# Performance work log

Hardware: AMD Instinct MI355X
Metric: run time of the kernel (lower is better)

Reference implementation:

```python
import jax, jax.numpy as jnp
import numpy as np

N_NODES = 100000
N_EDGES = 1600000
NFEAT = 128
NHID = 128
NCLASS = 40


def gcn_conv(x, W, b, src, dst, n_nodes):
    """PyG-style GCNConv: x' = D^{-1/2}(A+I)D^{-1/2} (x W) + b."""
    h = x @ W  # [N, out]
    loop = jnp.arange(n_nodes, dtype=src.dtype)
    s = jnp.concatenate([src, loop])  # add self-loops
    d = jnp.concatenate([dst, loop])
    deg = jax.ops.segment_sum(jnp.ones_like(s, dtype=h.dtype), d, num_segments=n_nodes)
    dinv = jnp.where(deg > 0, jax.lax.rsqrt(deg), 0.0)
    norm = dinv[s] * dinv[d]  # [E+N]
    msg = h[s] * norm[:, None]  # gather + scale
    out = jax.ops.segment_sum(msg, d, num_segments=n_nodes)  # scatter-add
    return out + b


def setup_inputs() -> dict:
    key = jax.random.key(0)
    ks = jax.random.split(key, 6)
    x = jax.random.normal(ks[0], (N_NODES, NFEAT), dtype=jnp.float32)
    edge_index = jax.random.randint(ks[1], (2, N_EDGES), 0, N_NODES, dtype=jnp.int64)
    sc1 = 1.0 / np.sqrt(NFEAT)
    sc2 = 1.0 / np.sqrt(NHID)
    W1 = jax.random.normal(ks[2], (NFEAT, NHID), dtype=jnp.float32) * sc1
    b1 = jnp.zeros((NHID,), dtype=jnp.float32)
    Wm = jax.random.normal(ks[3], (NHID, NHID), dtype=jnp.float32) * sc2
    bm = jnp.zeros((NHID,), dtype=jnp.float32)
    W2 = jax.random.normal(ks[4], (NHID, NCLASS), dtype=jnp.float32) * sc2
    b2 = jnp.zeros((NCLASS,), dtype=jnp.float32)
    return {"x": x, "edge_index": edge_index, "W1": W1, "b1": b1,
            "Wm": Wm, "bm": bm, "W2": W2, "b2": b2}


def reference(x, edge_index, W1, b1, Wm, bm, W2, b2):
    # StandGCNX forward, eval mode (dropout = identity)
    src, dst = edge_index[0], edge_index[1]
    n = x.shape[0]
    h = jax.nn.relu(gcn_conv(x, W1, b1, src, dst, n))
    h = jax.nn.relu(gcn_conv(h, Wm, bm, src, dst, n))
    out = gcn_conv(h, W2, b2, src, dst, n)
    return out
```

## Files before the change

kernel.cpp:

```cpp
#include <hip/hip_runtime.h>
#include <hip/hip_bf16.h>

typedef __attribute__((ext_vector_type(8))) short bf16x8;
typedef __attribute__((ext_vector_type(4))) float f32x4;

__device__ __forceinline__ ushort bf16rne(float f) {
    uint u = __float_as_uint(f);
    return (ushort)((u + 0x7fffu + ((u >> 16) & 1u)) >> 16);
}
__device__ __forceinline__ void unpack2(uint p, float& a, float& b) {
    a = __uint_as_float(p << 16);
    b = __uint_as_float(p & 0xffff0000u);
}


__global__ __launch_bounds__(256) void k_prep_pack(const float* __restrict__ W1,
                                                   const float* __restrict__ Wm,
                                                   const float* __restrict__ W2,
                                                   ushort* __restrict__ w1t,
                                                   ushort* __restrict__ wmt,
                                                   ushort* __restrict__ w2t,
                                                   const int* __restrict__ src,
                                                   const int* __restrict__ dst,
                                                   int* __restrict__ bcur,
                                                   uint* __restrict__ pairbuf,
                                                   int E, int nbuck, int CAP) {
    __shared__ int hist[512];
    __shared__ int scn[512];
    __shared__ int cur[512];
    __shared__ int gbase[512];
    __shared__ uint sorted[4096];
    int b = blockIdx.x;
    int t = threadIdx.x;
    if (b < 160) {
        if (b < 64) {
            int i = b * 256 + t; int k = i >> 7, n = i & 127;
            w1t[n * 128 + k] = bf16rne(W1[k * 128 + n]);
        } else if (b < 128) {
            int i = (b - 64) * 256 + t; int k = i >> 7, n = i & 127;
            wmt[n * 128 + k] = bf16rne(Wm[k * 128 + n]);
        } else {
            int i = (b - 128) * 256 + t;
            int n = i >> 7, k = i & 127;
            w2t[n * 128 + k] = (n < 40) ? bf16rne(W2[k * 40 + n]) : (ushort)0;
        }
        return;
    }
    int off = (b - 160) * 4096;
    int cnt = min(4096, E - off);
    hist[t] = 0; hist[t + 256] = 0;
    __syncthreads();
    for (int i = t; i < cnt; i += 256) {
        int bb = dst[off + i] >> 8;
        atomicAdd(&hist[bb], 1);
    }
    __syncthreads();
    scn[t] = hist[t]; scn[t + 256] = hist[t + 256];
    __syncthreads();
    for (int d = 1; d < 256; d <<= 1) {
        int u0 = (t >= d) ? scn[t - d] : 0;
        int u1 = (t >= d) ? scn[256 + t - d] : 0;
        __syncthreads();
        if (t >= d) { scn[t] += u0; scn[256 + t] += u1; }
        __syncthreads();
    }
    int tot0 = scn[255];
    scn[256 + t] += tot0;
    __syncthreads();
    cur[t] = (t == 0) ? 0 : scn[t - 1];
    cur[t + 256] = scn[t + 255];
    if (t < nbuck && hist[t] > 0)
        gbase[t] = t * CAP + atomicAdd(&bcur[t], hist[t]);
    int t2 = t + 256;
    if (t2 < nbuck && hist[t2] > 0)
        gbase[t2] = t2 * CAP + atomicAdd(&bcur[t2], hist[t2]);
    __syncthreads();
    for (int i = t; i < cnt; i += 256) {
        int d = dst[off + i];
        int s = src[off + i];
        int bb = d >> 8;
        int pos = atomicAdd(&cur[bb], 1);
        sorted[pos] = ((uint)(d & 255) << 24) | (uint)s;
    }
    __syncthreads();
    int wid = t >> 6, lane = t & 63;
    for (int bb = wid; bb < nbuck; bb += 4) {
        int n = hist[bb];
        if (n == 0) continue;
        int ls = (bb == 0) ? 0 : scn[bb - 1];
        int gb = gbase[bb];
        for (int j = lane; j < n; j += 64)
            pairbuf[gb + j] = sorted[ls + j];
    }
}


#define CSR_CAP 5632
__global__ __launch_bounds__(256) void k_csr_gemm(const uint* __restrict__ pairbuf,
                                                  const int* __restrict__ bcur,
                                                  int* __restrict__ rowptr,
                                                  int* __restrict__ rowend,
                                                  float* __restrict__ dinv,
                                                  int* __restrict__ csr,
                                                  int N, int nbuck, int CAP,
                                                  const float* __restrict__ A,
                                                  const ushort* __restrict__ Wt,
                                                  ushort* __restrict__ C, int M) {
    __shared__ int lhist[256];
    __shared__ int scn[256];
    __shared__ int lcur[256];
    __shared__ int lcsr[CSR_CAP];
    int t = threadIdx.x;
    if ((int)blockIdx.x >= nbuck) {
        int blk = blockIdx.x - nbuck;
        int wave = t >> 6, lane = t & 63;
        int m16 = lane & 15, quad = lane >> 4;
        int rowA = blk * 64 + wave * 16 + m16;
        int rA = min(rowA, M - 1);
        const float4* A4 = (const float4*)A;

        f32x4 acc[8];
#pragma unroll
        for (int i = 0; i < 8; i++) acc[i] = (f32x4){0.f, 0.f, 0.f, 0.f};
#pragma unroll
        for (int it = 0; it < 4; it++) {
            float4 f0 = A4[(size_t)rA * 32 + 8 * it + 2 * quad];
            float4 f1 = A4[(size_t)rA * 32 + 8 * it + 2 * quad + 1];
            bf16x8 af;
            af[0] = (short)bf16rne(f0.x); af[1] = (short)bf16rne(f0.y);
            af[2] = (short)bf16rne(f0.z); af[3] = (short)bf16rne(f0.w);
            af[4] = (short)bf16rne(f1.x); af[5] = (short)bf16rne(f1.y);
            af[6] = (short)bf16rne(f1.z); af[7] = (short)bf16rne(f1.w);
#pragma unroll
            for (int nt = 0; nt < 8; nt++) {
                bf16x8 bfr = *(const bf16x8*)(Wt + (size_t)(nt * 16 + m16) * 128 + it * 32 + quad * 8);
                acc[nt] = __builtin_amdgcn_mfma_f32_16x16x32_bf16(af, bfr, acc[nt], 0, 0, 0);
            }
        }
        int rowBase = blk * 64 + wave * 16 + quad * 4;
#pragma unroll
        for (int nt = 0; nt < 8; nt++) {
            int col = nt * 16 + m16;
#pragma unroll
            for (int r = 0; r < 4; r++) {
                int row = rowBase + r;
                if (row < M) C[(size_t)row * 128 + col] = bf16rne(acc[nt][r]);
            }
        }
        return;
    }
    int b = blockIdx.x;
    int base = b << 8;
    int nn = min(256, N - base);
    int lo = b * CAP;
    int cnt = bcur[b];
    lhist[t] = 0;
    __syncthreads();
    for (int i = t; i < cnt; i += 256) atomicAdd(&lhist[pairbuf[lo + i] >> 24], 1);
    __syncthreads();
    int mydeg = lhist[t];
    scn[t] = mydeg;
    __syncthreads();
    for (int d = 1; d < 256; d <<= 1) {
        int u = (t >= d) ? scn[t - d] : 0;
        __syncthreads();
        if (t >= d) scn[t] += u;
        __syncthreads();
    }
    int excl = (t == 0) ? 0 : scn[t - 1];
    lcur[t] = excl;
    if (t < nn) {
        rowptr[base + t] = lo + excl;
        rowend[base + t] = lo + excl + mydeg;
        dinv[base + t] = rsqrtf((float)(mydeg + 1));
    }
    __syncthreads();
    if (cnt <= CSR_CAP) {
        for (int i = t; i < cnt; i += 256) {
            uint p = pairbuf[lo + i];
            int pos = atomicAdd(&lcur[p >> 24], 1);
            lcsr[pos] = (int)(p & 0xFFFFFFu);
        }
        __syncthreads();
        for (int i = t; i < cnt; i += 256) csr[lo + i] = lcsr[i];
    } else {
        for (int i = t; i < cnt; i += 256) {
            uint p = pairbuf[lo + i];
            int pos = lo + atomicAdd(&lcur[p >> 24], 1);
            csr[pos] = (int)(p & 0xFFFFFFu);
        }
    }
}


template <bool EDGE_W>
__device__ __forceinline__ void batch8(const uint* __restrict__ g32, int lane,
                                       int creg, int wreg, int j, int lim,
                                       float& x0, float& x1) {
    uint P[8]; float W[8];
#pragma unroll
    for (int k = 0; k < 8; k++) {
        int idx = j + k;
        int cl = idx < 63 ? idx : 63;
        int s = __builtin_amdgcn_readlane(creg, cl);
        float w = EDGE_W ? __int_as_float(__builtin_amdgcn_readlane(wreg, cl)) : 1.0f;
        W[k] = (idx < lim) ? w : 0.0f;
        P[k] = g32[(size_t)s * 64 + lane];
    }
#pragma unroll
    for (int k = 0; k < 8; k++) {
        float u, v; unpack2(P[k], u, v);
        x0 += u * W[k]; x1 += v * W[k];
    }
}

template <bool EDGE_W>
__device__ __forceinline__ void batch8x2(const uint* __restrict__ g32, int lane,
                                         int cA, int wA, int jA, int limA,
                                         float& a0, float& a1,
                                         int cB, int wB, int jB, int limB,
                                         float& b0, float& b1) {
    uint PA[8], PB[8]; float WA[8], WB[8];
#pragma unroll
    for (int k = 0; k < 8; k++) {
        int idx = jA + k;
        int cl = idx < 63 ? idx : 63;
        int s = __builtin_amdgcn_readlane(cA, cl);
        float w = EDGE_W ? __int_as_float(__builtin_amdgcn_readlane(wA, cl)) : 1.0f;
        WA[k] = (idx < limA) ? w : 0.0f;
        PA[k] = g32[(size_t)s * 64 + lane];
    }
#pragma unroll
    for (int k = 0; k < 8; k++) {
        int idx = jB + k;
        int cl = idx < 63 ? idx : 63;
        int s = __builtin_amdgcn_readlane(cB, cl);
        float w = EDGE_W ? __int_as_float(__builtin_amdgcn_readlane(wB, cl)) : 1.0f;
        WB[k] = (idx < limB) ? w : 0.0f;
        PB[k] = g32[(size_t)s * 64 + lane];
    }
#pragma unroll
    for (int k = 0; k < 8; k++) {
        float u, v; unpack2(PA[k], u, v);
        a0 += u * WA[k]; a1 += v * WA[k];
    }
#pragma unroll
    for (int k = 0; k < 8; k++) {
        float u, v; unpack2(PB[k], u, v);
        b0 += u * WB[k]; b1 += v * WB[k];
    }
}

template <bool EDGE_W>
__device__ __forceinline__ void agg_node_chunked(const uint* __restrict__ g32,
                                                 const int* __restrict__ csr,
                                                 const float* __restrict__ dinv,
                                                 int lane, int e0, int e1,
                                                 float& x0, float& x1) {
    for (int base = e0; base < e1; base += 64) {
        int nc = e1 - base; if (nc > 64) nc = 64;
        int sidx = 0, swi = 0;
        if (lane < nc) {
            sidx = csr[base + lane];
            if (EDGE_W) swi = __float_as_int(dinv[sidx]);
        }
        int nc8 = (nc + 7) & ~7;
        for (int j = 0; j < nc8; j += 8)
            batch8<EDGE_W>(g32, lane, sidx, swi, j, nc, x0, x1);
    }
}

template <int NT, bool EDGE_W>
__device__ __forceinline__ void fused_agg_gemm(const ushort* __restrict__ g,
                                               const float* __restrict__ dinv,
                                               const int* __restrict__ rowptr,
                                               const int* __restrict__ rowend,
                                               const int* __restrict__ csr,
                                               const float* __restrict__ bias,
                                               const ushort* __restrict__ Wt,
                                               ushort* __restrict__ C,
                                               int M, int ccols) {
    __shared__ ushort hs[32][136];
    int t = threadIdx.x;
    int lane = t & 63;
    int wave = t >> 6;
    const uint* g32 = (const uint*)g;
    float2 bb = ((const float2*)bias)[lane];

    int nodeBase = blockIdx.x * 32 + wave * 8;
    int nd_l = min(nodeBase + lane, M - 1);

    uint srow[8];
#pragma unroll
    for (int i = 0; i < 8; i++) {
        int nd = __builtin_amdgcn_readlane(nd_l, i);
        srow[i] = g32[(size_t)nd * 64 + lane];
    }
    int e0_l = 0, e1_l = 0; float dn_l = 0.f;
    if (lane < 8) {
        e0_l = rowptr[nd_l];
        e1_l = rowend[nd_l];
        dn_l = dinv[nd_l];
    }
    int c0 = 0, c1 = 0, c2 = 0, c3 = 0;
    int w0 = 0, w1 = 0, w2 = 0, w3 = 0;
    int sp0, sp1, sp2, sp3, Ls0, Ls1, Ls2, Ls3;
    sp0 = __builtin_amdgcn_readlane(e0_l, 0);
    Ls0 = __builtin_amdgcn_readlane(e1_l, 1) - sp0;
    sp1 = __builtin_amdgcn_readlane(e0_l, 2);
    Ls1 = __builtin_amdgcn_readlane(e1_l, 3) - sp1;
    sp2 = __builtin_amdgcn_readlane(e0_l, 4);
    Ls2 = __builtin_amdgcn_readlane(e1_l, 5) - sp2;
    sp3 = __builtin_amdgcn_readlane(e0_l, 6);
    Ls3 = __builtin_amdgcn_readlane(e1_l, 7) - sp3;
    if (Ls0 > 0 && Ls0 <= 64 && lane < Ls0) c0 = csr[sp0 + lane];
    if (Ls1 > 0 && Ls1 <= 64 && lane < Ls1) c1 = csr[sp1 + lane];
    if (Ls2 > 0 && Ls2 <= 64 && lane < Ls2) c2 = csr[sp2 + lane];
    if (Ls3 > 0 && Ls3 <= 64 && lane < Ls3) c3 = csr[sp3 + lane];
    if (EDGE_W) {
        if (Ls0 > 0 && Ls0 <= 64 && lane < Ls0) w0 = __float_as_int(dinv[c0]);
        if (Ls1 > 0 && Ls1 <= 64 && lane < Ls1) w1 = __float_as_int(dinv[c1]);
        if (Ls2 > 0 && Ls2 <= 64 && lane < Ls2) w2 = __float_as_int(dinv[c2]);
        if (Ls3 > 0 && Ls3 <= 64 && lane < Ls3) w3 = __float_as_int(dinv[c3]);
    }
    int cp[4] = {c0, c1, c2, c3};
    int wp[4] = {w0, w1, w2, w3};
    int spp[4] = {sp0, sp1, sp2, sp3};
    int Lsp[4] = {Ls0, Ls1, Ls2, Ls3};

#pragma unroll
    for (int p = 0; p < 4; p++) {
        int iA = 2 * p, iB = 2 * p + 1;
        int eA0 = __builtin_amdgcn_readlane(e0_l, iA);
        int eA1 = __builtin_amdgcn_readlane(e1_l, iA);
        int eB0 = __builtin_amdgcn_readlane(e0_l, iB);
        int eB1 = __builtin_amdgcn_readlane(e1_l, iB);
        float dnA = __int_as_float(__builtin_amdgcn_readlane(__float_as_int(dn_l), iA));
        float dnB = __int_as_float(__builtin_amdgcn_readlane(__float_as_int(dn_l), iB));
        float a0, a1, b0, b1;
        {
            float u, v;
            unpack2(srow[2 * p], u, v);
            if (EDGE_W) { a0 = u * dnA; a1 = v * dnA; } else { a0 = u; a1 = v; }
            unpack2(srow[2 * p + 1], u, v);
            if (EDGE_W) { b0 = u * dnB; b1 = v * dnB; } else { b0 = u; b1 = v; }
        }
        if (Lsp[p] > 0 && Lsp[p] <= 64) {
            int offA = eA0 - spp[p];
            int offB = eB0 - spp[p];
            int nA = eA1 - eA0, nB = eB1 - eB0;
            int limA = offA + nA, limB = offB + nB;
            int jA = offA, jB = offB;
            int jAend = offA + ((nA + 7) & ~7);
            int jBend = offB + ((nB + 7) & ~7);
            while (jA < jAend && jB < jBend) {
                batch8x2<EDGE_W>(g32, lane, cp[p], wp[p], jA, limA, a0, a1,
                                 cp[p], wp[p], jB, limB, b0, b1);
                jA += 8; jB += 8;
            }
            while (jA < jAend) { batch8<EDGE_W>(g32, lane, cp[p], wp[p], jA, limA, a0, a1); jA += 8; }
            while (jB < jBend) { batch8<EDGE_W>(g32, lane, cp[p], wp[p], jB, limB, b0, b1); jB += 8; }
        } else if (Lsp[p] > 64) {
            agg_node_chunked<EDGE_W>(g32, csr, dinv, lane, eA0, eA1, a0, a1);
            agg_node_chunked<EDGE_W>(g32, csr, dinv, lane, eB0, eB1, b0, b1);
        }
        float o0 = fmaxf(a0 * dnA + bb.x, 0.f);
        float o1 = fmaxf(a1 * dnA + bb.y, 0.f);
        float o2 = fmaxf(b0 * dnB + bb.x, 0.f);
        float o3 = fmaxf(b1 * dnB + bb.y, 0.f);
        uint qA = (uint)bf16rne(o0) | ((uint)bf16rne(o1) << 16);
        uint qB = (uint)bf16rne(o2) | ((uint)bf16rne(o3) << 16);
        *(uint*)&hs[wave * 8 + 2 * p][lane * 2] = qA;
        *(uint*)&hs[wave * 8 + 2 * p + 1][lane * 2] = qB;
    }
    __syncthreads();

    int wv = t >> 6, lane6 = t & 63;
    int m16 = lane6 & 15, quad = lane6 >> 4;
    int rowHalf = wv & 1;
    int ntHalf = wv >> 1;
    constexpr int NTH = (NT + 1) / 2;
    int ntStart = ntHalf * NTH;
    int ntEnd = ntHalf ? NT : NTH;

    f32x4 acc[NTH];
#pragma unroll
    for (int i = 0; i < NTH; i++) acc[i] = (f32x4){0.f, 0.f, 0.f, 0.f};
#pragma unroll
    for (int it = 0; it < 4; it++) {
        bf16x8 af = *(const bf16x8*)&hs[rowHalf * 16 + m16][it * 32 + quad * 8];
        for (int nt = ntStart; nt < ntEnd; nt++) {
            bf16x8 bfr = *(const bf16x8*)(Wt + (size_t)(nt * 16 + m16) * 128 + it * 32 + quad * 8);
            acc[nt - ntStart] = __builtin_amdgcn_mfma_f32_16x16x32_bf16(af, bfr, acc[nt - ntStart], 0, 0, 0);
        }
    }
    int rowBase = blockIdx.x * 32 + rowHalf * 16 + quad * 4;
    float dnv[4];
#pragma unroll
    for (int r = 0; r < 4; r++) dnv[r] = dinv[min(rowBase + r, M - 1)];
    for (int nt = ntStart; nt < ntEnd; nt++) {
        int col = nt * 16 + m16;
        if (col >= ccols) continue;
#pragma unroll
        for (int r = 0; r < 4; r++) {
            int row = rowBase + r;
            if (row < M) C[(size_t)row * ccols + col] = bf16rne(acc[nt - ntStart][r] * dnv[r]);
        }
    }
}

__global__ __launch_bounds__(256) void k_fusedA(const ushort* __restrict__ g,
                                                const float* __restrict__ dinv,
                                                const int* __restrict__ rowptr,
                                                const int* __restrict__ rowend,
                                                const int* __restrict__ csr,
                                                const float* __restrict__ bias,
                                                const ushort* __restrict__ Wt,
                                                ushort* __restrict__ C, int M) {
    fused_agg_gemm<8, true>(g, dinv, rowptr, rowend, csr, bias, Wt, C, M, 128);
}

__global__ __launch_bounds__(256) void k_fusedB(const ushort* __restrict__ g,
                                                const float* __restrict__ dinv,
                                                const int* __restrict__ rowptr,
                                                const int* __restrict__ rowend,
                                                const int* __restrict__ csr,
                                                const float* __restrict__ bias,
                                                const ushort* __restrict__ Wt,
                                                ushort* __restrict__ C, int M) {
    fused_agg_gemm<4, false>(g, dinv, rowptr, rowend, csr, bias, Wt, C, M, 64);
}


__global__ __launch_bounds__(256) void k_agg40_b(const ushort* __restrict__ g3,
                                                 const float* __restrict__ dinv,
                                                 const int* __restrict__ rowptr,
                                                 const int* __restrict__ rowend,
                                                 const int* __restrict__ csr,
                                                 const float* __restrict__ bias,
                                                 float* __restrict__ out, int N) {
    int t = threadIdx.x;
    int wave = t >> 6, lane = t & 63;
    int half = lane >> 5, hl = lane & 31;
    const uint* gp = (const uint*)g3;

    int node0 = (blockIdx.x * 4 + wave) * 2;
    int nA = min(node0, N - 1);
    int nB = min(node0 + 1, N - 1);
    int myNode = half ? nB : nA;
    float dn = dinv[myNode];
    int e0A = rowptr[nA], e1A = rowend[nA];
    int e0B = rowptr[nB], e1B = rowend[nB];

    float a0, a1;
    {
        uint p = gp[(size_t)myNode * 32 + hl];
        unpack2(p, a0, a1);
    }
    int baseA = e0A, baseB = e0B;
    while (baseA < e1A || baseB < e1B) {
        int ncA = e1A - baseA; if (ncA > 32) ncA = 32; if (ncA < 0) ncA = 0;
        int ncB = e1B - baseB; if (ncB > 32) ncB = 32; if (ncB < 0) ncB = 0;
        int myBase = half ? baseB : baseA;
        int myNc = half ? ncB : ncA;
        int sidx = 0;
        if (hl < myNc) sidx = csr[myBase + hl];
        int lim = myNc;
        int m8A = (ncA + 7) & ~7;
        int m8B = (ncB + 7) & ~7;
        int m8 = m8A > m8B ? m8A : m8B;
        for (int j = 0; j < m8; j += 8) {
            uint P[8]; float W[8];
#pragma unroll
            for (int k = 0; k < 8; k++) {
                int idx = j + k;
                int cl = idx < 31 ? idx : 31;
                int sA = __builtin_amdgcn_readlane(sidx, cl);
                int sB = __builtin_amdgcn_readlane(sidx, 32 + cl);
                int s = half ? sB : sA;
                W[k] = (idx < lim) ? 1.0f : 0.0f;
                P[k] = gp[(size_t)s * 32 + hl];
            }
#pragma unroll
            for (int k = 0; k < 8; k++) {
                float u, v; unpack2(P[k], u, v);
                a0 += u * W[k]; a1 += v * W[k];
            }
        }
        baseA += ncA;
        baseB += ncB;
    }
    int onode = node0 + half;
    if (onode < N && hl < 20) {
        float2 bb = ((const float2*)bias)[hl];
        float2 o;
        o.x = a0 * dn + bb.x;
        o.y = a1 * dn + bb.y;
        ((float2*)out)[(size_t)onode * 20 + hl] = o;
    }
}


extern "C" void kernel_launch(void* const* d_in, const int* in_sizes, int n_in,
                              void* d_out, int out_size, void* d_ws, size_t ws_size,
                              hipStream_t stream) {
    const float* x  = (const float*)d_in[0];
    const int* eidx = (const int*)d_in[1];
    const float* W1 = (const float*)d_in[2];
    const float* b1 = (const float*)d_in[3];
    const float* Wm = (const float*)d_in[4];
    const float* bm = (const float*)d_in[5];
    const float* W2 = (const float*)d_in[6];
    const float* b2 = (const float*)d_in[7];
    float* out = (float*)d_out;

    int N = in_sizes[0] / 128;
    int E = in_sizes[1] / 2;
    const int* src = eidx;
    const int* dst = eidx + E;
    int nbuck = (N + 255) >> 8;
    int ntile = (E + 4095) / 4096;
    int CAP = ((E / nbuck) * 3 / 2 + 511) & ~511;

    char* ws = (char*)d_ws;
    size_t off = 0;
    auto alloc = [&](size_t bytes) -> void* {
        void* p = ws + off;
        off += (bytes + 255) & ~(size_t)255;
        return p;
    };
    float*  dinv    = (float*)alloc((size_t)N * 4);
    int*    rowptr  = (int*)alloc((size_t)N * 4);
    int*    rowend  = (int*)alloc((size_t)N * 4);
    int*    csr     = (int*)alloc((size_t)nbuck * CAP * 4);
    uint*   pairbuf = (uint*)alloc((size_t)nbuck * CAP * 4);
    int*    bcur    = (int*)alloc(512 * 4);
    ushort* w1t     = (ushort*)alloc(128 * 128 * 2);
    ushort* wmt     = (ushort*)alloc(128 * 128 * 2);
    ushort* w2t     = (ushort*)alloc(64 * 128 * 2);
    ushort* gbuf    = (ushort*)alloc((size_t)N * 128 * 2);
    ushort* gbuf2   = (ushort*)alloc((size_t)N * 128 * 2);
    ushort* g3      = (ushort*)alloc((size_t)N * 64 * 2);

    int gblk64 = (N + 63) / 64;
    int gblk32 = (N + 31) / 32;

    hipMemsetAsync(bcur, 0, 512 * 4, stream);
    k_prep_pack<<<160 + ntile, 256, 0, stream>>>(W1, Wm, W2, w1t, wmt, w2t,
                                                 src, dst, bcur, pairbuf, E, nbuck, CAP);
    k_csr_gemm<<<nbuck + gblk64, 256, 0, stream>>>(pairbuf, bcur, rowptr, rowend, dinv,
                                                   csr, N, nbuck, CAP, x, w1t, gbuf, N);
    k_fusedA<<<gblk32, 256, 0, stream>>>(gbuf, dinv, rowptr, rowend, csr, b1, wmt, gbuf2, N);
    k_fusedB<<<gblk32, 256, 0, stream>>>(gbuf2, dinv, rowptr, rowend, csr, bm, w2t, g3, N);
    k_agg40_b<<<(N + 7) / 8, 256, 0, stream>>>(g3, dinv, rowptr, rowend, csr, b2, out, N);
}
```

Measured before the change: 362.9 us.

## Prescale first GEMM output by source dinv to drop per-edge weights

Computes node degrees with global atomics during the edge bucketing pass and scales the first GEMM output rows by rsqrt(deg+1), so the layer-1 aggregation no longer needs to gather dinv per edge or multiply edge weights. Both fused aggregation kernels now use the unweighted path. This removes a random dinv gather and readlane per edge in layer 1, at the cost of 1.6M global atomics on deg and a larger memset.

New measurement: 418.1 us. 1.15x slower.

```diff
diff --git a/kernel.cpp b/kernel.cpp
--- a/kernel.cpp
+++ b/kernel.cpp
@@ -23,6 +23,7 @@
                                                    const int* __restrict__ src,
                                                    const int* __restrict__ dst,
                                                    int* __restrict__ bcur,
+                                                   int* __restrict__ deg,
                                                    uint* __restrict__ pairbuf,
                                                    int E, int nbuck, int CAP) {
     __shared__ int hist[512];
@@ -78,6 +79,7 @@
     for (int i = t; i < cnt; i += 256) {
         int d = dst[off + i];
         int s = src[off + i];
+        atomicAdd(&deg[d], 1);
         int bb = d >> 8;
         int pos = atomicAdd(&cur[bb], 1);
         sorted[pos] = ((uint)(d & 255) << 24) | (uint)s;
@@ -98,6 +100,7 @@
 #define CSR_CAP 5632
 __global__ __launch_bounds__(256) void k_csr_gemm(const uint* __restrict__ pairbuf,
                                                   const int* __restrict__ bcur,
+                                                  const int* __restrict__ deg,
                                                   int* __restrict__ rowptr,
                                                   int* __restrict__ rowend,
                                                   float* __restrict__ dinv,
@@ -138,13 +141,17 @@
             }
         }
         int rowBase = blk * 64 + wave * 16 + quad * 4;
+        float dnr[4];
+#pragma unroll
+        for (int r = 0; r < 4; r++)
+            dnr[r] = rsqrtf((float)(deg[min(rowBase + r, M - 1)] + 1));
 #pragma unroll
         for (int nt = 0; nt < 8; nt++) {
             int col = nt * 16 + m16;
 #pragma unroll
             for (int r = 0; r < 4; r++) {
                 int row = rowBase + r;
-                if (row < M) C[(size_t)row * 128 + col] = bf16rne(acc[nt][r]);
+                if (row < M) C[(size_t)row * 128 + col] = bf16rne(acc[nt][r] * dnr[r]);
             }
         }
         return;
@@ -193,9 +200,8 @@
 }
 
 
-template <bool EDGE_W>
 __device__ __forceinline__ void batch8(const uint* __restrict__ g32, int lane,
-                                       int creg, int wreg, int j, int lim,
+                                       int creg, int j, int lim,
                                        float& x0, float& x1) {
     uint P[8]; float W[8];
 #pragma unroll
@@ -203,8 +209,7 @@
         int idx = j + k;
         int cl = idx < 63 ? idx : 63;
         int s = __builtin_amdgcn_readlane(creg, cl);
-        float w = EDGE_W ? __int_as_float(__builtin_amdgcn_readlane(wreg, cl)) : 1.0f;
-        W[k] = (idx < lim) ? w : 0.0f;
+        W[k] = (idx < lim) ? 1.0f : 0.0f;
         P[k] = g32[(size_t)s * 64 + lane];
     }
 #pragma unroll
@@ -214,11 +219,10 @@
     }
 }
 
-template <bool EDGE_W>
 __device__ __forceinline__ void batch8x2(const uint* __restrict__ g32, int lane,
-                                         int cA, int wA, int jA, int limA,
+                                         int cA, int jA, int limA,
                                          float& a0, float& a1,
-                                         int cB, int wB, int jB, int limB,
+                                         int cB, int jB, int limB,
                                          float& b0, float& b1) {
     uint PA[8], PB[8]; float WA[8], WB[8];
 #pragma unroll
@@ -226,8 +230,7 @@
         int idx = jA + k;
         int cl = idx < 63 ? idx : 63;
         int s = __builtin_amdgcn_readlane(cA, cl);
-        float w = EDGE_W ? __int_as_float(__builtin_amdgcn_readlane(wA, cl)) : 1.0f;
-        WA[k] = (idx < limA) ? w : 0.0f;
+        WA[k] = (idx < limA) ? 1.0f : 0.0f;
         PA[k] = g32[(size_t)s * 64 + lane];
     }
 #pragma unroll
@@ -235,8 +238,7 @@
         int idx = jB + k;
         int cl = idx < 63 ? idx : 63;
         int s = __builtin_amdgcn_readlane(cB, cl);
-        float w = EDGE_W ? __int_as_float(__builtin_amdgcn_readlane(wB, cl)) : 1.0f;
-        WB[k] = (idx < limB) ? w : 0.0f;
+        WB[k] = (idx < limB) ? 1.0f : 0.0f;
         PB[k] = g32[(size_t)s * 64 + lane];
     }
 #pragma unroll
@@ -251,26 +253,21 @@
     }
 }
 
-template <bool EDGE_W>
 __device__ __forceinline__ void agg_node_chunked(const uint* __restrict__ g32,
                                                  const int* __restrict__ csr,
-                                                 const float* __restrict__ dinv,
                                                  int lane, int e0, int e1,
                                                  float& x0, float& x1) {
     for (int base = e0; base < e1; base += 64) {
         int nc = e1 - base; if (nc > 64) nc = 64;
-        int sidx = 0, swi = 0;
-        if (lane < nc) {
-            sidx = csr[base + lane];
-            if (EDGE_W) swi = __float_as_int(dinv[sidx]);
-        }
+        int sidx = 0;
+        if (lane < nc) sidx = csr[base + lane];
         int nc8 = (nc + 7) & ~7;
         for (int j = 0; j < nc8; j += 8)
-            batch8<EDGE_W>(g32, lane, sidx, swi, j, nc, x0, x1);
-    }
-}
-
-template <int NT, bool EDGE_W>
+            batch8(g32, lane, sidx, j, nc, x0, x1);
+    }
+}
+
+template <int NT>
 __device__ __forceinline__ void fused_agg_gemm(const ushort* __restrict__ g,
                                                const float* __restrict__ dinv,
                                                const int* __restrict__ rowptr,
@@ -303,7 +300,6 @@
         dn_l = dinv[nd_l];
     }
     int c0 = 0, c1 = 0, c2 = 0, c3 = 0;
-    int w0 = 0, w1 = 0, w2 = 0, w3 = 0;
     int sp0, sp1, sp2, sp3, Ls0, Ls1, Ls2, Ls3;
     sp0 = __builtin_amdgcn_readlane(e0_l, 0);
     Ls0 = __builtin_amdgcn_readlane(e1_l, 1) - sp0;
@@ -317,14 +313,7 @@
     if (Ls1 > 0 && Ls1 <= 64 && lane < Ls1) c1 = csr[sp1 + lane];
     if (Ls2 > 0 && Ls2 <= 64 && lane < Ls2) c2 = csr[sp2 + lane];
     if (Ls3 > 0 && Ls3 <= 64 && lane < Ls3) c3 = csr[sp3 + lane];
-    if (EDGE_W) {
-        if (Ls0 > 0 && Ls0 <= 64 && lane < Ls0) w0 = __float_as_int(dinv[c0]);
-        if (Ls1 > 0 && Ls1 <= 64 && lane < Ls1) w1 = __float_as_int(dinv[c1]);
-        if (Ls2 > 0 && Ls2 <= 64 && lane < Ls2) w2 = __float_as_int(dinv[c2]);
-        if (Ls3 > 0 && Ls3 <= 64 && lane < Ls3) w3 = __float_as_int(dinv[c3]);
-    }
     int cp[4] = {c0, c1, c2, c3};
-    int wp[4] = {w0, w1, w2, w3};
     int spp[4] = {sp0, sp1, sp2, sp3};
     int Lsp[4] = {Ls0, Ls1, Ls2, Ls3};
 
@@ -341,9 +330,9 @@
         {
             float u, v;
             unpack2(srow[2 * p], u, v);
-            if (EDGE_W) { a0 = u * dnA; a1 = v * dnA; } else { a0 = u; a1 = v; }
+            a0 = u; a1 = v;
             unpack2(srow[2 * p + 1], u, v);
-            if (EDGE_W) { b0 = u * dnB; b1 = v * dnB; } else { b0 = u; b1 = v; }
+            b0 = u; b1 = v;
         }
         if (Lsp[p] > 0 && Lsp[p] <= 64) {
             int offA = eA0 - spp[p];
@@ -354,15 +343,15 @@
             int jAend = offA + ((nA + 7) & ~7);
             int jBend = offB + ((nB + 7) & ~7);
             while (jA < jAend && jB < jBend) {
-                batch8x2<EDGE_W>(g32, lane, cp[p], wp[p], jA, limA, a0, a1,
-                                 cp[p], wp[p], jB, limB, b0, b1);
+                batch8x2(g32, lane, cp[p], jA, limA, a0, a1,
+                         cp[p], jB, limB, b0, b1);
                 jA += 8; jB += 8;
             }
-            while (jA < jAend) { batch8<EDGE_W>(g32, lane, cp[p], wp[p], jA, limA, a0, a1); jA += 8; }
-            while (jB < jBend) { batch8<EDGE_W>(g32, lane, cp[p], wp[p], jB, limB, b0, b1); jB += 8; }
+            while (jA < jAend) { batch8(g32, lane, cp[p], jA, limA, a0, a1); jA += 8; }
+            while (jB < jBend) { batch8(g32, lane, cp[p], jB, limB, b0, b1); jB += 8; }
         } else if (Lsp[p] > 64) {
-            agg_node_chunked<EDGE_W>(g32, csr, dinv, lane, eA0, eA1, a0, a1);
-            agg_node_chunked<EDGE_W>(g32, csr, dinv, lane, eB0, eB1, b0, b1);
+            agg_node_chunked(g32, csr, lane, eA0, eA1, a0, a1);
+            agg_node_chunked(g32, csr, lane, eB0, eB1, b0, b1);
         }
         float o0 = fmaxf(a0 * dnA + bb.x, 0.f);
         float o1 = fmaxf(a1 * dnA + bb.y, 0.f);
@@ -417,7 +406,7 @@
                                                 const float* __restrict__ bias,
                                                 const ushort* __restrict__ Wt,
                                                 ushort* __restrict__ C, int M) {
-    fused_agg_gemm<8, true>(g, dinv, rowptr, rowend, csr, bias, Wt, C, M, 128);
+    fused_agg_gemm<8>(g, dinv, rowptr, rowend, csr, bias, Wt, C, M, 128);
 }
 
 __global__ __launch_bounds__(256) void k_fusedB(const ushort* __restrict__ g,
@@ -428,7 +417,7 @@
                                                 const float* __restrict__ bias,
                                                 const ushort* __restrict__ Wt,
                                                 ushort* __restrict__ C, int M) {
-    fused_agg_gemm<4, false>(g, dinv, rowptr, rowend, csr, bias, Wt, C, M, 64);
+    fused_agg_gemm<4>(g, dinv, rowptr, rowend, csr, bias, Wt, C, M, 64);
 }
 
 
@@ -529,12 +518,13 @@
         off += (bytes + 255) & ~(size_t)255;
         return p;
     };
+    int*    bcur    = (int*)alloc(512 * 4);
+    int*    deg     = (int*)alloc((size_t)N * 4);
     float*  dinv    = (float*)alloc((size_t)N * 4);
     int*    rowptr  = (int*)alloc((size_t)N * 4);
     int*    rowend  = (int*)alloc((size_t)N * 4);
     int*    csr     = (int*)alloc((size_t)nbuck * CAP * 4);
     uint*   pairbuf = (uint*)alloc((size_t)nbuck * CAP * 4);
-    int*    bcur    = (int*)alloc(512 * 4);
     ushort* w1t     = (ushort*)alloc(128 * 128 * 2);
     ushort* wmt     = (ushort*)alloc(128 * 128 * 2);
     ushort* w2t     = (ushort*)alloc(64 * 128 * 2);
@@ -545,10 +535,10 @@
     int gblk64 = (N + 63) / 64;
     int gblk32 = (N + 31) / 32;
 
-    hipMemsetAsync(bcur, 0, 512 * 4, stream);
+    hipMemsetAsync(bcur, 0, 512 * 4 + (size_t)N * 4, stream);
     k_prep_pack<<<160 + ntile, 256, 0, stream>>>(W1, Wm, W2, w1t, wmt, w2t,
-                                                 src, dst, bcur, pairbuf, E, nbuck, CAP);
-    k_csr_gemm<<<nbuck + gblk64, 256, 0, stream>>>(pairbuf, bcur, rowptr, rowend, dinv,
+                                                 src, dst, bcur, deg, pairbuf, E, nbuck, CAP);
+    k_csr_gemm<<<nbuck + gblk64, 256, 0, stream>>>(pairbuf, bcur, deg, rowptr, rowend, dinv,
                                                    csr, N, nbuck, CAP, x, w1t, gbuf, N);
     k_fusedA<<<gblk32, 256, 0, stream>>>(gbuf, dinv, rowptr, rowend, csr, b1, wmt, gbuf2, N);
     k_fusedB<<<gblk32, 256, 0, stream>>>(gbuf2, dinv, rowptr, rowend, csr, bm, w2t, g3, N);
```

## Halve bucket tile, pad bucket counters, and flatten scatter copy-out loop

Applied to the files above, without the earlier changes.

Halves the per-block edge tile used for bucketing, which doubles the number of blocks and cuts shared memory per block. Pads each bucket's global atomic counter to its own 64-byte slot to avoid contention and false sharing between neighbouring buckets. Replaces the per-wave, per-bucket copy-out loop with a flat per-element loop that uses a shared bucket-id lookup array. The flat loop gives better load balance, but each thread now writes its bucket's range of the lookup array serially, and the smaller tiles double the number of global atomics on the counters.

After: 363.4 us. About the same (+0.1%).

```diff
diff --git a/kernel.cpp b/kernel.cpp
--- a/kernel.cpp
+++ b/kernel.cpp
@@ -12,6 +12,8 @@
     a = __uint_as_float(p << 16);
     b = __uint_as_float(p & 0xffff0000u);
 }
+
+#define TILE 2048
 
 
 __global__ __launch_bounds__(256) void k_prep_pack(const float* __restrict__ W1,
@@ -29,7 +31,8 @@
     __shared__ int scn[512];
     __shared__ int cur[512];
     __shared__ int gbase[512];
-    __shared__ uint sorted[4096];
+    __shared__ uint sorted[TILE];
+    __shared__ ushort posb[TILE];
     int b = blockIdx.x;
     int t = threadIdx.x;
     if (b < 160) {
@@ -46,8 +49,8 @@
         }
         return;
     }
-    int off = (b - 160) * 4096;
-    int cnt = min(4096, E - off);
+    int off = (b - 160) * TILE;
+    int cnt = min(TILE, E - off);
     hist[t] = 0; hist[t + 256] = 0;
     __syncthreads();
     for (int i = t; i < cnt; i += 256) {
@@ -70,10 +73,10 @@
     cur[t] = (t == 0) ? 0 : scn[t - 1];
     cur[t + 256] = scn[t + 255];
     if (t < nbuck && hist[t] > 0)
-        gbase[t] = t * CAP + atomicAdd(&bcur[t], hist[t]);
+        gbase[t] = t * CAP + atomicAdd(&bcur[t * 16], hist[t]);
     int t2 = t + 256;
     if (t2 < nbuck && hist[t2] > 0)
-        gbase[t2] = t2 * CAP + atomicAdd(&bcur[t2], hist[t2]);
+        gbase[t2] = t2 * CAP + atomicAdd(&bcur[t2 * 16], hist[t2]);
     __syncthreads();
     for (int i = t; i < cnt; i += 256) {
         int d = dst[off + i];
@@ -83,14 +86,19 @@
         sorted[pos] = ((uint)(d & 255) << 24) | (uint)s;
     }
     __syncthreads();
-    int wid = t >> 6, lane = t & 63;
-    for (int bb = wid; bb < nbuck; bb += 4) {
-        int n = hist[bb];
-        if (n == 0) continue;
-        int ls = (bb == 0) ? 0 : scn[bb - 1];
-        int gb = gbase[bb];
-        for (int j = lane; j < n; j += 64)
-            pairbuf[gb + j] = sorted[ls + j];
+    {
+        int ls = (t == 0) ? 0 : scn[t - 1];
+        int le = scn[t];
+        for (int i = ls; i < le; i++) posb[i] = (ushort)t;
+        int ls2 = scn[t2 - 1];
+        int le2 = scn[t2];
+        for (int i = ls2; i < le2; i++) posb[i] = (ushort)t2;
+    }
+    __syncthreads();
+    for (int i = t; i < cnt; i += 256) {
+        int bb = posb[i];
+        int lsb = (bb == 0) ? 0 : scn[bb - 1];
+        pairbuf[gbase[bb] + (i - lsb)] = sorted[i];
     }
 }
 
@@ -153,7 +161,7 @@
     int base = b << 8;
     int nn = min(256, N - base);
     int lo = b * CAP;
-    int cnt = bcur[b];
+    int cnt = bcur[b * 16];
     lhist[t] = 0;
     __syncthreads();
     for (int i = t; i < cnt; i += 256) atomicAdd(&lhist[pairbuf[lo + i] >> 24], 1);
@@ -519,7 +527,7 @@
     const int* src = eidx;
     const int* dst = eidx + E;
     int nbuck = (N + 255) >> 8;
-    int ntile = (E + 4095) / 4096;
+    int ntile = (E + TILE - 1) / TILE;
     int CAP = ((E / nbuck) * 3 / 2 + 511) & ~511;
 
     char* ws = (char*)d_ws;
@@ -529,12 +537,12 @@
         off += (bytes + 255) & ~(size_t)255;
         return p;
     };
+    int*    bcur    = (int*)alloc(512 * 16 * 4);
     float*  dinv    = (float*)alloc((size_t)N * 4);
     int*    rowptr  = (int*)alloc((size_t)N * 4);
     int*    rowend  = (int*)alloc((size_t)N * 4);
     int*    csr     = (int*)alloc((size_t)nbuck * CAP * 4);
     uint*   pairbuf = (uint*)alloc((size_t)nbuck * CAP * 4);
-    int*    bcur    = (int*)alloc(512 * 4);
     ushort* w1t     = (ushort*)alloc(128 * 128 * 2);
     ushort* wmt     = (ushort*)alloc(128 * 128 * 2);
     ushort* w2t     = (ushort*)alloc(64 * 128 * 2);
@@ -545,7 +553,7 @@
     int gblk64 = (N + 63) / 64;
     int gblk32 = (N + 31) / 32;
 
-    hipMemsetAsync(bcur, 0, 512 * 4, stream);
+    hipMemsetAsync(bcur, 0, 512 * 16 * 4, stream);
     k_prep_pack<<<160 + ntile, 256, 0, stream>>>(W1, Wm, W2, w1t, wmt, w2t,
                                                  src, dst, bcur, pairbuf, E, nbuck, CAP);
     k_csr_gemm<<<nbuck + gblk64, 256, 0, stream>>>(pairbuf, bcur, rowptr, rowend, dinv,
```
